# Kernel optimization log

Hardware: AMD Instinct MI355X
Metric: run time of the kernel (lower is better)

## Reference

```python
import jax, jax.numpy as jnp
import numpy as np

D_INPUT = 2048
DD_DIM = 512
DD_PAIRS = DD_DIM // 2


def setup_inputs() -> dict:
    key = jax.random.key(0)
    k1, k2, k3 = jax.random.split(key, 3)
    x = jax.random.normal(k1, (4, 4096, D_INPUT), dtype=jnp.float32)
    # Learned projection (zeros at init in torch; use small random for a non-trivial test)
    W = jax.random.normal(k2, (DD_PAIRS, D_INPUT), dtype=jnp.float32) * 0.02
    b = jax.random.normal(k3, (DD_PAIRS,), dtype=jnp.float32) * 0.02
    return {"x": x, "W": W, "b": b}


def reference(x, W, b):
    # x: (B, T, D); W: (P, D); b: (P,) with P = DD_DIM // 2
    deltas = jnp.einsum('btd,pd->btp', x, W) + b          # (B, T, P)
    angles = jnp.cumsum(deltas, axis=1)                   # cumulative phase
    cos, sin = jnp.cos(angles), jnp.sin(angles)
    x1 = x[..., :DD_PAIRS]                                # (B, T, P)
    x2 = x[..., DD_PAIRS:DD_DIM]                          # (B, T, P)
    rotated = jnp.concatenate([x1 * cos - x2 * sin, x2 * cos + x1 * sin], axis=-1)
    return jnp.concatenate([rotated, x[..., DD_DIM:]], axis=-1)
```

## Files before the change

### kernel.cpp

```cpp
#include <hip/hip_runtime.h>
#include <math.h>

#define BB 4
#define TT 4096
#define DDIM 2048
#define PP 256
#define MM (BB*TT)
#define KKDIM 2048
#define CHUNK 32
#define NCHUNK (TT/CHUNK)

typedef __attribute__((ext_vector_type(8))) short short8;
typedef __attribute__((ext_vector_type(4))) float f32x4;

__device__ __forceinline__ unsigned short f2bf(float f) {
    unsigned u = __float_as_uint(f);
    u += 0x7FFF + ((u >> 16) & 1);
    return (unsigned short)(u >> 16);
}
__device__ __forceinline__ float bf2f(unsigned short h) {
    return __uint_as_float(((unsigned)h) << 16);
}

#define LSTR 56

__global__ __launch_bounds__(256) void gemm_mfma_k(const float* __restrict__ x,
                                                   const float* __restrict__ W,
                                                   const float* __restrict__ bias,
                                                   float* __restrict__ delta,
                                                   float* __restrict__ csum) {
    __shared__ unsigned short Ahi[128 * LSTR];
    __shared__ unsigned short Alo[128 * LSTR];
    __shared__ unsigned short Bhi[64 * LSTR];
    __shared__ unsigned short Blo[64 * LSTR];

    const int n0   = blockIdx.x * 64;
    const int m0   = blockIdx.y * 128;
    const int tid  = threadIdx.x;
    const int w    = tid >> 6;
    const int lane = tid & 63;
    const int lm   = lane & 15;
    const int ko   = lane >> 4;

    f32x4 acc[2][4];
    #pragma unroll
    for (int i = 0; i < 2; ++i)
        #pragma unroll
        for (int j = 0; j < 4; ++j) {
            f32x4 z = {0.f, 0.f, 0.f, 0.f};
            acc[i][j] = z;
        }

    for (int k0 = 0; k0 < KKDIM; k0 += 32) {
        float4 av[4], bv[2];
        #pragma unroll
        for (int r = 0; r < 4; ++r) {
            int f = r * 256 + tid;
            av[r] = *(const float4*)(x + (size_t)(m0 + (f >> 3)) * KKDIM + k0 + ((f & 7) << 2));
        }
        #pragma unroll
        for (int r = 0; r < 2; ++r) {
            int f = r * 256 + tid;
            bv[r] = *(const float4*)(W + (size_t)(n0 + (f >> 3)) * KKDIM + k0 + ((f & 7) << 2));
        }
        __syncthreads();
        #pragma unroll
        for (int r = 0; r < 4; ++r) {
            int f = r * 256 + tid;
            int idx = (f >> 3) * LSTR + ((f & 7) << 2);
            float4 v = av[r];
            unsigned short h0 = f2bf(v.x), h1 = f2bf(v.y), h2 = f2bf(v.z), h3 = f2bf(v.w);
            unsigned short l0 = f2bf(v.x - bf2f(h0)), l1 = f2bf(v.y - bf2f(h1));
            unsigned short l2 = f2bf(v.z - bf2f(h2)), l3 = f2bf(v.w - bf2f(h3));
            uint2 hp = { (unsigned)h0 | ((unsigned)h1 << 16), (unsigned)h2 | ((unsigned)h3 << 16) };
            uint2 lp = { (unsigned)l0 | ((unsigned)l1 << 16), (unsigned)l2 | ((unsigned)l3 << 16) };
            *(uint2*)&Ahi[idx] = hp;
            *(uint2*)&Alo[idx] = lp;
        }
        #pragma unroll
        for (int r = 0; r < 2; ++r) {
            int f = r * 256 + tid;
            int idx = (f >> 3) * LSTR + ((f & 7) << 2);
            float4 v = bv[r];
            unsigned short h0 = f2bf(v.x), h1 = f2bf(v.y), h2 = f2bf(v.z), h3 = f2bf(v.w);
            unsigned short l0 = f2bf(v.x - bf2f(h0)), l1 = f2bf(v.y - bf2f(h1));
            unsigned short l2 = f2bf(v.z - bf2f(h2)), l3 = f2bf(v.w - bf2f(h3));
            uint2 hp = { (unsigned)h0 | ((unsigned)h1 << 16), (unsigned)h2 | ((unsigned)h3 << 16) };
            uint2 lp = { (unsigned)l0 | ((unsigned)l1 << 16), (unsigned)l2 | ((unsigned)l3 << 16) };
            *(uint2*)&Bhi[idx] = hp;
            *(uint2*)&Blo[idx] = lp;
        }
        __syncthreads();
        short8 ah[2], al[2], bh[4], bl[4];
        #pragma unroll
        for (int mt = 0; mt < 2; ++mt) {
            int idx = (w * 32 + mt * 16 + lm) * LSTR + ko * 8;
            ah[mt] = *(const short8*)&Ahi[idx];
            al[mt] = *(const short8*)&Alo[idx];
        }
        #pragma unroll
        for (int nt = 0; nt < 4; ++nt) {
            int idx = (nt * 16 + lm) * LSTR + ko * 8;
            bh[nt] = *(const short8*)&Bhi[idx];
            bl[nt] = *(const short8*)&Blo[idx];
        }
        #pragma unroll
        for (int mt = 0; mt < 2; ++mt)
            #pragma unroll
            for (int nt = 0; nt < 4; ++nt) {
                f32x4 c = acc[mt][nt];
                c = __builtin_amdgcn_mfma_f32_16x16x32_bf16(ah[mt], bh[nt], c, 0, 0, 0);
                c = __builtin_amdgcn_mfma_f32_16x16x32_bf16(ah[mt], bl[nt], c, 0, 0, 0);
                c = __builtin_amdgcn_mfma_f32_16x16x32_bf16(al[mt], bh[nt], c, 0, 0, 0);
                acc[mt][nt] = c;
            }
    }

    float bsv[4];
    #pragma unroll
    for (int nt = 0; nt < 4; ++nt) bsv[nt] = bias[n0 + nt * 16 + lm];

    float cs[4] = {0.f, 0.f, 0.f, 0.f};
    #pragma unroll
    for (int mt = 0; mt < 2; ++mt)
        #pragma unroll
        for (int nt = 0; nt < 4; ++nt)
            #pragma unroll
            for (int r = 0; r < 4; ++r) {
                float val = acc[mt][nt][r] + bsv[nt];
                int m = m0 + w * 32 + mt * 16 + ko * 4 + r;
                delta[(size_t)m * PP + n0 + nt * 16 + lm] = val;
                cs[nt] += val;
            }
    #pragma unroll
    for (int nt = 0; nt < 4; ++nt) {
        float s = cs[nt];
        s += __shfl_xor(s, 16);
        s += __shfl_xor(s, 32);
        if (lane < 16)
            csum[(size_t)(m0 / CHUNK + w) * PP + n0 + nt * 16 + lane] = s;
    }
}

__global__ __launch_bounds__(256) void scan_k(float* __restrict__ csum, int cstride) {
    const int idx = blockIdx.x * 256 + threadIdx.x;
    const int b = idx >> 8;
    const int p = idx & 255;
    float run = 0.f;
    for (int c0 = 0; c0 < NCHUNK; c0 += 8) {
        float v[8];
        #pragma unroll
        for (int j = 0; j < 8; ++j)
            v[j] = csum[(size_t)(b * NCHUNK + c0 + j) * cstride + p];
        #pragma unroll
        for (int j = 0; j < 8; ++j) {
            float t = v[j];
            csum[(size_t)(b * NCHUNK + c0 + j) * cstride + p] = run;
            run += t;
        }
    }
}

__global__ __launch_bounds__(256) void rotate_copy_k(const float* __restrict__ delta,
                                                     const float* __restrict__ csum,
                                                     const float* __restrict__ x,
                                                     float* __restrict__ out) {
    const int bc = blockIdx.x;
    const int p  = threadIdx.x;
    const int tbase = bc * CHUNK;
    float angle = csum[(size_t)bc * PP + p];
    for (int t = 0; t < CHUNK; ++t) {
        size_t row = (size_t)(tbase + t);
        angle += delta[row * PP + p];
        float s, co;
        sincosf(angle, &s, &co);
        float x1 = x[row * DDIM + p];
        float x2 = x[row * DDIM + PP + p];
        out[row * DDIM + p]      = x1 * co - x2 * s;
        out[row * DDIM + PP + p] = x2 * co + x1 * s;
    }
    const int half = p >> 7;
    const int q    = p & 127;
    for (int rp = 0; rp < 16; ++rp) {
        size_t row = (size_t)(tbase + rp * 2 + half);
        const float4* src = (const float4*)(x + row * DDIM + 512);
        float4*       dst = (float4*)(out + row * DDIM + 512);
        dst[q]       = src[q];
        dst[q + 128] = src[q + 128];
        dst[q + 256] = src[q + 256];
    }
}

__global__ __launch_bounds__(256) void gemm_k(const float* __restrict__ x,
                                              const float* __restrict__ W,
                                              const float* __restrict__ bias,
                                              float* __restrict__ delta,
                                              int dstride, int doff) {
    __shared__ float As[16][68];
    __shared__ float Bs[16][68];
    const int m0  = blockIdx.x * 64;
    const int n0  = blockIdx.y * 64;
    const int tid = threadIdx.x;
    const int lr  = tid >> 2;
    const int lc  = (tid & 3) << 2;
    const int tmi = tid & 15;
    const int tni = tid >> 4;
    float acc[4][4] = {};
    for (int k0 = 0; k0 < KKDIM; k0 += 16) {
        float4 a4 = *(const float4*)(x + (size_t)(m0 + lr) * KKDIM + k0 + lc);
        float4 b4 = *(const float4*)(W + (size_t)(n0 + lr) * KKDIM + k0 + lc);
        __syncthreads();
        As[lc + 0][lr] = a4.x; As[lc + 1][lr] = a4.y;
        As[lc + 2][lr] = a4.z; As[lc + 3][lr] = a4.w;
        Bs[lc + 0][lr] = b4.x; Bs[lc + 1][lr] = b4.y;
        Bs[lc + 2][lr] = b4.z; Bs[lc + 3][lr] = b4.w;
        __syncthreads();
        #pragma unroll
        for (int kk = 0; kk < 16; ++kk) {
            float4 av = *(const float4*)&As[kk][tmi * 4];
            float4 bv = *(const float4*)&Bs[kk][tni * 4];
            float am[4] = {av.x, av.y, av.z, av.w};
            float bn[4] = {bv.x, bv.y, bv.z, bv.w};
            #pragma unroll
            for (int i = 0; i < 4; ++i)
                #pragma unroll
                for (int j = 0; j < 4; ++j)
                    acc[i][j] += am[i] * bn[j];
        }
    }
    const float4 b4 = *(const float4*)(bias + n0 + tni * 4);
    #pragma unroll
    for (int i = 0; i < 4; ++i) {
        size_t m = (size_t)(m0 + tmi * 4 + i);
        float4 o;
        o.x = acc[i][0] + b4.x; o.y = acc[i][1] + b4.y;
        o.z = acc[i][2] + b4.z; o.w = acc[i][3] + b4.w;
        *(float4*)(delta + m * dstride + doff + n0 + tni * 4) = o;
    }
}

__global__ __launch_bounds__(256) void chunksum_k(const float* __restrict__ delta,
                                                  int dstride, int doff,
                                                  float* __restrict__ csum, int cstride) {
    const int bc = blockIdx.x;
    const int b  = bc / NCHUNK;
    const int c  = bc % NCHUNK;
    const int p  = threadIdx.x;
    const int tbase = b * TT + c * CHUNK;
    float s = 0.f;
    #pragma unroll 8
    for (int t = 0; t < CHUNK; ++t)
        s += delta[(size_t)(tbase + t) * dstride + doff + p];
    csum[(size_t)bc * cstride + p] = s;
}

__global__ __launch_bounds__(256) void rotate_k(const float* __restrict__ delta,
                                                int dstride, int doff,
                                                const float* __restrict__ csum, int cstride,
                                                const float* __restrict__ x,
                                                float* __restrict__ out) {
    const int bc = blockIdx.x;
    const int b  = bc / NCHUNK;
    const int c  = bc % NCHUNK;
    const int p  = threadIdx.x;
    const int tbase = b * TT + c * CHUNK;
    float angle = csum[(size_t)bc * cstride + p];
    for (int t = 0; t < CHUNK; ++t) {
        size_t row = (size_t)(tbase + t);
        angle += delta[row * dstride + doff + p];
        float s, co;
        sincosf(angle, &s, &co);
        float x1 = x[row * DDIM + p];
        float x2 = x[row * DDIM + PP + p];
        out[row * DDIM + p]      = x1 * co - x2 * s;
        out[row * DDIM + PP + p] = x2 * co + x1 * s;
    }
}

__global__ __launch_bounds__(256) void copy_k(const float* __restrict__ x,
                                              float* __restrict__ out) {
    const size_t row = (size_t)blockIdx.x * 4 + (threadIdx.x >> 6);
    const int lane = threadIdx.x & 63;
    const int col = 512 + (blockIdx.y * 64 + lane) * 4;
    const size_t a = row * DDIM + col;
    *(float4*)(out + a) = *(const float4*)(x + a);
}

extern "C" void kernel_launch(void* const* d_in, const int* in_sizes, int n_in,
                              void* d_out, int out_size, void* d_ws, size_t ws_size,
                              hipStream_t stream) {
    const float* x    = (const float*)d_in[0];
    const float* W    = (const float*)d_in[1];
    const float* bias = (const float*)d_in[2];
    float* out = (float*)d_out;

    const size_t delta_elems = (size_t)MM * PP;
    const size_t csum_elems  = (size_t)BB * NCHUNK * PP;
    const size_t need = (delta_elems + csum_elems) * sizeof(float);

    if (ws_size >= need) {
        float* delta = (float*)d_ws;
        float* csum  = (float*)d_ws + delta_elems;
        gemm_mfma_k<<<dim3(PP / 64, MM / 128), 256, 0, stream>>>(x, W, bias, delta, csum);
        scan_k<<<(BB * PP) / 256, 256, 0, stream>>>(csum, PP);
        rotate_copy_k<<<BB * NCHUNK, 256, 0, stream>>>(delta, csum, x, out);
    } else {
        float* delta = out; const int dstride = DDIM, doff = 512;
        float* csum  = out + 768; const int cstride = DDIM;
        gemm_k<<<dim3(MM / 64, PP / 64), 256, 0, stream>>>(x, W, bias, delta, dstride, doff);
        chunksum_k<<<BB * NCHUNK, 256, 0, stream>>>(delta, dstride, doff, csum, cstride);
        scan_k<<<(BB * PP) / 256, 256, 0, stream>>>(csum, cstride);
        rotate_k<<<BB * NCHUNK, 256, 0, stream>>>(delta, dstride, doff, csum, cstride, x, out);
        copy_k<<<dim3(MM / 4, 6), 256, 0, stream>>>(x, out);
    }
}
```

Before: 364.5 us.

## Precompute split-bf16 W, load GEMM operands directly to registers, fuse copy and scan

Adds a kernel that splits W into bf16 hi/lo halves once. The GEMM is rewritten to load x and the pre-split W straight from global memory into MFMA fragment registers with software prefetching, so shared memory and barriers are no longer needed. The n-block-0 tiles write the untouched x columns to the output inside the GEMM, and block indices are swizzled for L2 locality. The separate scan kernel is removed; each rotate block sums the preceding chunk totals itself. This trades redundant prefix reads and uncoalesced per-lane global loads for fewer launches and no LDS traffic.

```diff
diff --git a/kernel.cpp b/kernel.cpp
--- a/kernel.cpp
+++ b/kernel.cpp
@@ -22,26 +22,64 @@
     return __uint_as_float(((unsigned)h) << 16);
 }
 
-#define LSTR 56
-
-__global__ __launch_bounds__(256) void gemm_mfma_k(const float* __restrict__ x,
-                                                   const float* __restrict__ W,
-                                                   const float* __restrict__ bias,
-                                                   float* __restrict__ delta,
-                                                   float* __restrict__ csum) {
-    __shared__ unsigned short Ahi[128 * LSTR];
-    __shared__ unsigned short Alo[128 * LSTR];
-    __shared__ unsigned short Bhi[64 * LSTR];
-    __shared__ unsigned short Blo[64 * LSTR];
-
-    const int n0   = blockIdx.x * 64;
-    const int m0   = blockIdx.y * 128;
+__device__ __forceinline__ void cvt8(const float4& va, const float4& vb,
+                                     short8& hi, short8& lo) {
+    float f[8] = {va.x, va.y, va.z, va.w, vb.x, vb.y, vb.z, vb.w};
+    #pragma unroll
+    for (int j = 0; j < 8; ++j) {
+        unsigned short h = f2bf(f[j]);
+        hi[j] = (short)h;
+        lo[j] = (short)f2bf(f[j] - bf2f(h));
+    }
+}
+
+__global__ __launch_bounds__(256) void prep_w_k(const float* __restrict__ W,
+                                                unsigned short* __restrict__ Whi,
+                                                unsigned short* __restrict__ Wlo) {
+    const int i = blockIdx.x * 256 + threadIdx.x;
+    float4 v = ((const float4*)W)[i];
+    unsigned short h0 = f2bf(v.x), h1 = f2bf(v.y), h2 = f2bf(v.z), h3 = f2bf(v.w);
+    unsigned short l0 = f2bf(v.x - bf2f(h0)), l1 = f2bf(v.y - bf2f(h1));
+    unsigned short l2 = f2bf(v.z - bf2f(h2)), l3 = f2bf(v.w - bf2f(h3));
+    uint2 hp = { (unsigned)h0 | ((unsigned)h1 << 16), (unsigned)h2 | ((unsigned)h3 << 16) };
+    uint2 lp = { (unsigned)l0 | ((unsigned)l1 << 16), (unsigned)l2 | ((unsigned)l3 << 16) };
+    *(uint2*)&Whi[(size_t)i * 4] = hp;
+    *(uint2*)&Wlo[(size_t)i * 4] = lp;
+}
+
+__global__ __launch_bounds__(256, 2) void gemm_mfma2_k(const float* __restrict__ x,
+                                                       const unsigned short* __restrict__ Whi,
+                                                       const unsigned short* __restrict__ Wlo,
+                                                       const float* __restrict__ bias,
+                                                       float* __restrict__ delta,
+                                                       float* __restrict__ csum,
+                                                       float* __restrict__ out) {
+    const int hw      = blockIdx.y * 4 + blockIdx.x;
+    const int logical = (hw & 7) * 64 + (hw >> 3);
+    const int nidx    = logical & 3;
+    const int midx    = logical >> 2;
+    const int n0      = nidx * 64;
+    const int m0      = midx * 128;
+    const bool docopy = (nidx == 0);
+
     const int tid  = threadIdx.x;
     const int w    = tid >> 6;
     const int lane = tid & 63;
     const int lm   = lane & 15;
     const int ko   = lane >> 4;
 
+    const int rowA = m0 + w * 32 + lm;
+    const float* xr0 = x + (size_t)rowA * KKDIM + ko * 8;
+    const float* xr1 = xr0 + (size_t)16 * KKDIM;
+    const unsigned short* wh[4];
+    const unsigned short* wl[4];
+    #pragma unroll
+    for (int nt = 0; nt < 4; ++nt) {
+        size_t off = (size_t)(n0 + nt * 16 + lm) * KKDIM + ko * 8;
+        wh[nt] = Whi + off;
+        wl[nt] = Wlo + off;
+    }
+
     f32x4 acc[2][4];
     #pragma unroll
     for (int i = 0; i < 2; ++i)
@@ -51,69 +89,56 @@
             acc[i][j] = z;
         }
 
+    float4 aC0 = *(const float4*)(xr0);
+    float4 aC1 = *(const float4*)(xr0 + 4);
+    float4 aC2 = *(const float4*)(xr1);
+    float4 aC3 = *(const float4*)(xr1 + 4);
+    short8 bhC[4], blC[4];
+    #pragma unroll
+    for (int nt = 0; nt < 4; ++nt) {
+        bhC[nt] = *(const short8*)(wh[nt]);
+        blC[nt] = *(const short8*)(wl[nt]);
+    }
+
     for (int k0 = 0; k0 < KKDIM; k0 += 32) {
-        float4 av[4], bv[2];
-        #pragma unroll
-        for (int r = 0; r < 4; ++r) {
-            int f = r * 256 + tid;
-            av[r] = *(const float4*)(x + (size_t)(m0 + (f >> 3)) * KKDIM + k0 + ((f & 7) << 2));
-        }
-        #pragma unroll
-        for (int r = 0; r < 2; ++r) {
-            int f = r * 256 + tid;
-            bv[r] = *(const float4*)(W + (size_t)(n0 + (f >> 3)) * KKDIM + k0 + ((f & 7) << 2));
-        }
-        __syncthreads();
-        #pragma unroll
-        for (int r = 0; r < 4; ++r) {
-            int f = r * 256 + tid;
-            int idx = (f >> 3) * LSTR + ((f & 7) << 2);
-            float4 v = av[r];
-            unsigned short h0 = f2bf(v.x), h1 = f2bf(v.y), h2 = f2bf(v.z), h3 = f2bf(v.w);
-            unsigned short l0 = f2bf(v.x - bf2f(h0)), l1 = f2bf(v.y - bf2f(h1));
-            unsigned short l2 = f2bf(v.z - bf2f(h2)), l3 = f2bf(v.w - bf2f(h3));
-            uint2 hp = { (unsigned)h0 | ((unsigned)h1 << 16), (unsigned)h2 | ((unsigned)h3 << 16) };
-            uint2 lp = { (unsigned)l0 | ((unsigned)l1 << 16), (unsigned)l2 | ((unsigned)l3 << 16) };
-            *(uint2*)&Ahi[idx] = hp;
-            *(uint2*)&Alo[idx] = lp;
-        }
-        #pragma unroll
-        for (int r = 0; r < 2; ++r) {
-            int f = r * 256 + tid;
-            int idx = (f >> 3) * LSTR + ((f & 7) << 2);
-            float4 v = bv[r];
-            unsigned short h0 = f2bf(v.x), h1 = f2bf(v.y), h2 = f2bf(v.z), h3 = f2bf(v.w);
-            unsigned short l0 = f2bf(v.x - bf2f(h0)), l1 = f2bf(v.y - bf2f(h1));
-            unsigned short l2 = f2bf(v.z - bf2f(h2)), l3 = f2bf(v.w - bf2f(h3));
-            uint2 hp = { (unsigned)h0 | ((unsigned)h1 << 16), (unsigned)h2 | ((unsigned)h3 << 16) };
-            uint2 lp = { (unsigned)l0 | ((unsigned)l1 << 16), (unsigned)l2 | ((unsigned)l3 << 16) };
-            *(uint2*)&Bhi[idx] = hp;
-            *(uint2*)&Blo[idx] = lp;
-        }
-        __syncthreads();
-        short8 ah[2], al[2], bh[4], bl[4];
-        #pragma unroll
-        for (int mt = 0; mt < 2; ++mt) {
-            int idx = (w * 32 + mt * 16 + lm) * LSTR + ko * 8;
-            ah[mt] = *(const short8*)&Ahi[idx];
-            al[mt] = *(const short8*)&Alo[idx];
-        }
+        const int kn = (k0 + 32 < KKDIM) ? (k0 + 32) : k0;
+        float4 aN0 = *(const float4*)(xr0 + kn);
+        float4 aN1 = *(const float4*)(xr0 + kn + 4);
+        float4 aN2 = *(const float4*)(xr1 + kn);
+        float4 aN3 = *(const float4*)(xr1 + kn + 4);
+        short8 bhN[4], blN[4];
         #pragma unroll
         for (int nt = 0; nt < 4; ++nt) {
-            int idx = (nt * 16 + lm) * LSTR + ko * 8;
-            bh[nt] = *(const short8*)&Bhi[idx];
-            bl[nt] = *(const short8*)&Blo[idx];
-        }
-        #pragma unroll
-        for (int mt = 0; mt < 2; ++mt)
-            #pragma unroll
-            for (int nt = 0; nt < 4; ++nt) {
-                f32x4 c = acc[mt][nt];
-                c = __builtin_amdgcn_mfma_f32_16x16x32_bf16(ah[mt], bh[nt], c, 0, 0, 0);
-                c = __builtin_amdgcn_mfma_f32_16x16x32_bf16(ah[mt], bl[nt], c, 0, 0, 0);
-                c = __builtin_amdgcn_mfma_f32_16x16x32_bf16(al[mt], bh[nt], c, 0, 0, 0);
-                acc[mt][nt] = c;
-            }
+            bhN[nt] = *(const short8*)(wh[nt] + kn);
+            blN[nt] = *(const short8*)(wl[nt] + kn);
+        }
+        short8 ah0, al0, ah1, al1;
+        cvt8(aC0, aC1, ah0, al0);
+        cvt8(aC2, aC3, ah1, al1);
+        if (docopy && k0 >= 512) {
+            float* o0 = out + (size_t)rowA * DDIM + k0 + ko * 8;
+            float* o1 = o0 + (size_t)16 * DDIM;
+            *(float4*)o0       = aC0;
+            *(float4*)(o0 + 4) = aC1;
+            *(float4*)o1       = aC2;
+            *(float4*)(o1 + 4) = aC3;
+        }
+        #pragma unroll
+        for (int nt = 0; nt < 4; ++nt) {
+            f32x4 c0 = acc[0][nt];
+            c0 = __builtin_amdgcn_mfma_f32_16x16x32_bf16(ah0, bhC[nt], c0, 0, 0, 0);
+            c0 = __builtin_amdgcn_mfma_f32_16x16x32_bf16(ah0, blC[nt], c0, 0, 0, 0);
+            c0 = __builtin_amdgcn_mfma_f32_16x16x32_bf16(al0, bhC[nt], c0, 0, 0, 0);
+            acc[0][nt] = c0;
+            f32x4 c1 = acc[1][nt];
+            c1 = __builtin_amdgcn_mfma_f32_16x16x32_bf16(ah1, bhC[nt], c1, 0, 0, 0);
+            c1 = __builtin_amdgcn_mfma_f32_16x16x32_bf16(ah1, blC[nt], c1, 0, 0, 0);
+            c1 = __builtin_amdgcn_mfma_f32_16x16x32_bf16(al1, bhC[nt], c1, 0, 0, 0);
+            acc[1][nt] = c1;
+        }
+        aC0 = aN0; aC1 = aN1; aC2 = aN2; aC3 = aN3;
+        #pragma unroll
+        for (int nt = 0; nt < 4; ++nt) { bhC[nt] = bhN[nt]; blC[nt] = blN[nt]; }
     }
 
     float bsv[4];
@@ -142,33 +167,28 @@
     }
 }
 
-__global__ __launch_bounds__(256) void scan_k(float* __restrict__ csum, int cstride) {
-    const int idx = blockIdx.x * 256 + threadIdx.x;
-    const int b = idx >> 8;
-    const int p = idx & 255;
-    float run = 0.f;
-    for (int c0 = 0; c0 < NCHUNK; c0 += 8) {
-        float v[8];
-        #pragma unroll
-        for (int j = 0; j < 8; ++j)
-            v[j] = csum[(size_t)(b * NCHUNK + c0 + j) * cstride + p];
-        #pragma unroll
-        for (int j = 0; j < 8; ++j) {
-            float t = v[j];
-            csum[(size_t)(b * NCHUNK + c0 + j) * cstride + p] = run;
-            run += t;
-        }
-    }
-}
-
-__global__ __launch_bounds__(256) void rotate_copy_k(const float* __restrict__ delta,
-                                                     const float* __restrict__ csum,
-                                                     const float* __restrict__ x,
-                                                     float* __restrict__ out) {
+__global__ __launch_bounds__(256) void rotate2_k(const float* __restrict__ delta,
+                                                 const float* __restrict__ csum,
+                                                 const float* __restrict__ x,
+                                                 float* __restrict__ out) {
     const int bc = blockIdx.x;
+    const int c  = bc & (NCHUNK - 1);
+    const int b  = bc >> 7;
     const int p  = threadIdx.x;
+
+    const float* cs = csum + (size_t)(b * NCHUNK) * PP + p;
+    float angle = 0.f;
+    int c0 = 0;
+    for (; c0 + 16 <= c; c0 += 16) {
+        float v[16];
+        #pragma unroll
+        for (int j = 0; j < 16; ++j) v[j] = cs[(size_t)(c0 + j) * PP];
+        #pragma unroll
+        for (int j = 0; j < 16; ++j) angle += v[j];
+    }
+    for (; c0 < c; ++c0) angle += cs[(size_t)c0 * PP];
+
     const int tbase = bc * CHUNK;
-    float angle = csum[(size_t)bc * PP + p];
     for (int t = 0; t < CHUNK; ++t) {
         size_t row = (size_t)(tbase + t);
         angle += delta[row * PP + p];
@@ -178,16 +198,6 @@
         float x2 = x[row * DDIM + PP + p];
         out[row * DDIM + p]      = x1 * co - x2 * s;
         out[row * DDIM + PP + p] = x2 * co + x1 * s;
-    }
-    const int half = p >> 7;
-    const int q    = p & 127;
-    for (int rp = 0; rp < 16; ++rp) {
-        size_t row = (size_t)(tbase + rp * 2 + half);
-        const float4* src = (const float4*)(x + row * DDIM + 512);
-        float4*       dst = (float4*)(out + row * DDIM + 512);
-        dst[q]       = src[q];
-        dst[q + 128] = src[q + 128];
-        dst[q + 256] = src[q + 256];
     }
 }
 
@@ -254,16 +264,33 @@
     csum[(size_t)bc * cstride + p] = s;
 }
 
+__global__ __launch_bounds__(256) void scan_k(float* __restrict__ csum, int cstride) {
+    const int idx = blockIdx.x * 256 + threadIdx.x;
+    const int b = idx >> 8;
+    const int p = idx & 255;
+    float run = 0.f;
+    for (int c0 = 0; c0 < NCHUNK; c0 += 8) {
+        float v[8];
+        #pragma unroll
+        for (int j = 0; j < 8; ++j)
+            v[j] = csum[(size_t)(b * NCHUNK + c0 + j) * cstride + p];
+        #pragma unroll
+        for (int j = 0; j < 8; ++j) {
+            float t = v[j];
+            csum[(size_t)(b * NCHUNK + c0 + j) * cstride + p] = run;
+            run += t;
+        }
+    }
+}
+
 __global__ __launch_bounds__(256) void rotate_k(const float* __restrict__ delta,
                                                 int dstride, int doff,
                                                 const float* __restrict__ csum, int cstride,
                                                 const float* __restrict__ x,
                                                 float* __restrict__ out) {
     const int bc = blockIdx.x;
-    const int b  = bc / NCHUNK;
-    const int c  = bc % NCHUNK;
     const int p  = threadIdx.x;
-    const int tbase = b * TT + c * CHUNK;
+    const int tbase = bc * CHUNK;
     float angle = csum[(size_t)bc * cstride + p];
     for (int t = 0; t < CHUNK; ++t) {
         size_t row = (size_t)(tbase + t);
@@ -296,14 +323,19 @@
 
     const size_t delta_elems = (size_t)MM * PP;
     const size_t csum_elems  = (size_t)BB * NCHUNK * PP;
-    const size_t need = (delta_elems + csum_elems) * sizeof(float);
+    const size_t w_elems     = (size_t)PP * KKDIM;
+    const size_t need = (delta_elems + csum_elems) * sizeof(float)
+                      + 2 * w_elems * sizeof(unsigned short);
 
     if (ws_size >= need) {
         float* delta = (float*)d_ws;
         float* csum  = (float*)d_ws + delta_elems;
-        gemm_mfma_k<<<dim3(PP / 64, MM / 128), 256, 0, stream>>>(x, W, bias, delta, csum);
-        scan_k<<<(BB * PP) / 256, 256, 0, stream>>>(csum, PP);
-        rotate_copy_k<<<BB * NCHUNK, 256, 0, stream>>>(delta, csum, x, out);
+        unsigned short* Whi = (unsigned short*)(csum + csum_elems);
+        unsigned short* Wlo = Whi + w_elems;
+        prep_w_k<<<(PP * KKDIM / 4) / 256, 256, 0, stream>>>(W, Whi, Wlo);
+        gemm_mfma2_k<<<dim3(4, MM / 128), 256, 0, stream>>>(x, Whi, Wlo, bias,
+                                                            delta, csum, out);
+        rotate2_k<<<BB * NCHUNK, 256, 0, stream>>>(delta, csum, x, out);
     } else {
         float* delta = out; const int dstride = DDIM, doff = 512;
         float* csum  = out + 768; const int cstride = DDIM;
```

Result: slower. 416.9 us (+14.4%).
